# Optimization experiments

Hardware: AMD Instinct MI355X
Metric: run time of the kernel (lower is better)

Reference implementation:

```python
import jax, jax.numpy as jnp
from jax import lax
import numpy as np

D_MODEL, D_STATE, D_CONV, EXPAND = 192, 16, 3, 2
D_INNER = EXPAND * D_MODEL
B_, H_, W_ = 8, 128, 128
PAD = (D_CONV - 1) // 2
EPS = 1e-5


def setup_inputs() -> dict:
    key = jax.random.key(0)
    ks = jax.random.split(key, 8)
    s = 0.02
    return {
        "x": jax.random.normal(ks[0], (B_, D_MODEL, H_, W_), jnp.float32),
        "w_in": jax.random.normal(ks[1], (D_MODEL, 2 * D_INNER), jnp.float32) * s,
        "w_conv": jax.random.normal(ks[2], (D_INNER, 1, D_CONV, D_CONV), jnp.float32) * s,
        "b_conv": jnp.zeros((D_INNER,), jnp.float32),
        "w_x": jax.random.normal(ks[3], (D_INNER, 2 * D_STATE), jnp.float32) * s,
        "w_dt": jax.random.normal(ks[4], (D_STATE, D_INNER), jnp.float32) * s,
        "b_dt": jnp.zeros((D_INNER,), jnp.float32),
        "D_skip": jnp.ones((D_INNER,), jnp.float32),
        "w_out": jax.random.normal(ks[5], (D_INNER, D_MODEL), jnp.float32) * s,
        "gamma": jnp.ones((D_INNER,), jnp.float32),
        "beta": jnp.zeros((D_INNER,), jnp.float32),
    }


def _ss2d(x, w_in, w_conv, b_conv, w_x, w_dt, b_dt, D_skip, w_out, gamma, beta):
    B, C, H, W = x.shape
    L = H * W
    # NOTE: faithful to torch: x.reshape(B, H*W, C) on an NCHW tensor is a raw
    # row-major reinterpretation (same semantics as jnp.reshape), not a transpose.
    x_flat = x.reshape(B, L, C)
    x_proj = x_flat @ w_in                     # [B, L, 2*d_inner]
    x_inner, z = jnp.split(x_proj, 2, axis=-1)
    # depthwise conv over spatial dims
    xc = jnp.transpose(x_inner, (0, 2, 1)).reshape(B, D_INNER, H, W)
    xc = lax.conv_general_dilated(
        xc, w_conv, window_strides=(1, 1), padding=[(PAD, PAD), (PAD, PAD)],
        dimension_numbers=("NCHW", "OIHW", "NCHW"), feature_group_count=D_INNER,
    ) + b_conv[None, :, None, None]
    xc = jax.nn.silu(xc)
    xc = jnp.transpose(xc.reshape(B, D_INNER, L), (0, 2, 1))   # [B, L, d_inner]
    x_ssm = xc @ w_x                                            # [B, L, 2*d_state]
    B_ssm, C_ssm = jnp.split(x_ssm, 2, axis=-1)
    dt = jax.nn.softplus(B_ssm @ w_dt + b_dt)                   # [B, L, d_inner]
    # Original: deltaB = dt[...,None]*B_ssm[:,:,None,:]; einsum('blid,bld->bli', deltaB, C_ssm)
    # == dt * sum_d(B_ssm*C_ssm)  (deltaA is computed but never used -> dropped)
    bc = jnp.sum(B_ssm * C_ssm, axis=-1, keepdims=True)         # [B, L, 1]
    y = dt * bc + xc * D_skip                                   # [B, L, d_inner]
    y = y * jax.nn.silu(z)
    mu = jnp.mean(y, axis=-1, keepdims=True)
    var = jnp.mean(jnp.square(y - mu), axis=-1, keepdims=True)
    y = (y - mu) * lax.rsqrt(var + EPS) * gamma + beta
    out = y @ w_out                                             # [B, L, d_model]
    return jnp.transpose(out, (0, 2, 1)).reshape(B, C, H, W)


def reference(x, w_in, w_conv, b_conv, w_x, w_dt, b_dt, D_skip, w_out, gamma, beta):
    return _ss2d(x, w_in, w_conv, b_conv, w_x, w_dt, b_dt, D_skip, w_out, gamma, beta)
```

## Files before the change

kernel.cpp:

```cpp
#include <hip/hip_runtime.h>
#include <hip/hip_bf16.h>

typedef __bf16 bf16x8 __attribute__((ext_vector_type(8)));
typedef __bf16 bf16x4 __attribute__((ext_vector_type(4)));
typedef float  f32x4  __attribute__((ext_vector_type(4)));

__device__ __forceinline__ f32x4 mfma16(bf16x8 a, bf16x8 b, f32x4 c) {
    return __builtin_amdgcn_mfma_f32_16x16x32_bf16(a, b, c, 0, 0, 0);
}
__device__ __forceinline__ float silu_f(float v) { return v / (1.f + __expf(-v)); }
__device__ __forceinline__ float softplus_fast(float v) {
    float r = __logf(1.f + __expf(v));
    return v > 15.f ? v : r;
}

#define CC 192
#define DI 384
#define LL 16384
#define HH 128
#define WW 128

__global__ void k0_prep(const float* __restrict__ w_in, const float* __restrict__ w_x,
                        const float* __restrict__ w_dt, const float* __restrict__ w_out,
                        __bf16* __restrict__ wt_in, __bf16* __restrict__ wt_x,
                        __bf16* __restrict__ wt_dt, __bf16* __restrict__ wt_out) {
    int tid = blockIdx.x * blockDim.x + threadIdx.x;
    int nth = gridDim.x * blockDim.x;
    for (int i = tid; i < 768 * 192; i += nth) { int n = i / 192, k = i % 192; wt_in[i] = (__bf16)w_in[k * 768 + n]; }
    for (int i = tid; i < 32 * 384;  i += nth) { int n = i / 384, k = i % 384; wt_x[i]  = (__bf16)w_x[k * 32 + n]; }
    for (int i = tid; i < 384 * 16;  i += nth) { int ch = i / 16, k = i % 16;  wt_dt[i] = (__bf16)w_dt[k * 384 + ch]; }
    for (int i = tid; i < 192 * 384; i += nth) { int n = i / 384, k = i % 384; wt_out[i] = (__bf16)w_out[k * 192 + n]; }
}

__global__ __launch_bounds__(256, 4) void k1_proj(
        const float* __restrict__ x, const __bf16* __restrict__ wt_in,
        __bf16* __restrict__ xin, __bf16* __restrict__ zsb) {
    __shared__ __attribute__((aligned(16))) __bf16 wb[4 * 2 * 32 * 68];
    const int tid = threadIdx.x;
    const int lane = tid & 63, wv = tid >> 6;
    const int lq = lane & 15, quad = lane >> 4;
    const long mbase = (long)blockIdx.x * 128;
    __bf16* wbase = wb + wv * (2 * 32 * 68);

    bf16x8 af[2][6];
#pragma unroll
    for (int mt = 0; mt < 2; mt++) {
        const float* xr = x + (mbase + wv * 32 + mt * 16 + lq) * CC;
#pragma unroll
        for (int ks = 0; ks < 6; ks++) {
            float4 v0 = *(const float4*)(xr + ks * 32 + quad * 8);
            float4 v1 = *(const float4*)(xr + ks * 32 + quad * 8 + 4);
            bf16x8 t;
            t[0] = (__bf16)v0.x; t[1] = (__bf16)v0.y; t[2] = (__bf16)v0.z; t[3] = (__bf16)v0.w;
            t[4] = (__bf16)v1.x; t[5] = (__bf16)v1.y; t[6] = (__bf16)v1.z; t[7] = (__bf16)v1.w;
            af[mt][ks] = t;
        }
    }

    for (int nc = 0; nc < 12; nc++) {
        const __bf16* bnc = wt_in + (long)(nc * 64 + lq) * CC + quad * 8;
        f32x4 A0[4], A1[4];
#pragma unroll
        for (int nt = 0; nt < 4; nt++) {
            A0[nt] = (f32x4){0.f, 0.f, 0.f, 0.f};
            A1[nt] = (f32x4){0.f, 0.f, 0.f, 0.f};
        }
        bf16x8 bp[6];
#pragma unroll
        for (int i = 0; i < 6; i++)
            bp[i] = *(const bf16x8*)(bnc + (long)(i / 6) * 16 * CC + (i % 6) * 32);
#pragma unroll
        for (int i = 0; i < 24; i++) {
            const int nt = i / 6, ks = i % 6;
            bf16x8 bcur = bp[i % 6];
            const int i2 = i + 6;
            if (i2 < 24)
                bp[i % 6] = *(const bf16x8*)(bnc + (long)(i2 / 6) * 16 * CC + (i2 % 6) * 32);
            A0[nt] = mfma16(af[0][ks], bcur, A0[nt]);
            A1[nt] = mfma16(af[1][ks], bcur, A1[nt]);
        }
        const bool isz = (nc >= 6);
        __bf16* bb = wbase + (nc & 1) * (32 * 68);
#pragma unroll
        for (int nt = 0; nt < 4; nt++) {
#pragma unroll
            for (int r = 0; r < 4; r++) {
                float v0 = A0[nt][r], v1 = A1[nt][r];
                if (isz) { v0 = silu_f(v0); v1 = silu_f(v1); }
                bb[(quad * 4 + r) * 68 + nt * 16 + lq] = (__bf16)v0;
                bb[(16 + quad * 4 + r) * 68 + nt * 16 + lq] = (__bf16)v1;
            }
        }
        __builtin_amdgcn_wave_barrier();
        __bf16* dst = isz ? zsb : xin;
        const int chb = (isz ? nc - 6 : nc) * 64;
#pragma unroll
        for (int k = 0; k < 4; k++) {
            int u = lane + k * 64;
            int row = u >> 3, c8 = u & 7;
            unsigned long long lo = *(const unsigned long long*)(&bb[row * 68 + c8 * 8]);
            unsigned long long hi = *(const unsigned long long*)(&bb[row * 68 + c8 * 8 + 4]);
            ulonglong2 val; val.x = lo; val.y = hi;
            *(ulonglong2*)(dst + (mbase + wv * 32 + row) * DI + chb + c8 * 8) = val;
        }
        __builtin_amdgcn_wave_barrier();
    }
}

__global__ __launch_bounds__(256, 2) void k3_ssm(
        const __bf16* __restrict__ xin, const __bf16* __restrict__ zsb,
        const __bf16* __restrict__ wtx, const __bf16* __restrict__ wtdt,
        const __bf16* __restrict__ wtout, const float* __restrict__ wconv,
        const float* __restrict__ bconv, const float* __restrict__ bdt,
        const float* __restrict__ dskip, const float* __restrict__ gamma,
        const float* __restrict__ beta, float* __restrict__ out) {
    __shared__ __attribute__((aligned(16))) float smem0[13056];
    __shared__ __attribute__((aligned(16))) __bf16 dts[64 * 200];
    __shared__ __attribute__((aligned(16))) __bf16 bss[64 * 24];
    __shared__ float bcarr[64];
    __bf16* xcb = (__bf16*)smem0;
    float* otile = smem0;

    const int tid = threadIdx.x;
    const int lane = tid & 63, wv = tid >> 6;
    const int lq = lane & 15, quad = lane >> 4;
    const int t0g = blockIdx.x * 64;

    const int te = tid >> 2, part = tid & 3;
    const long tok = t0g + te;

    bf16x8 zpre[12];
#pragma unroll
    for (int h = 0; h < 2; h++)
#pragma unroll
        for (int g = 0; g < 6; g++)
            zpre[h * 6 + g] = *(const bf16x8*)(zsb + tok * DI + h * 192 + part * 48 + g * 8);

    float* wcvs = (float*)dts;
    float* bcvs = wcvs + 9 * 384;
    for (int u = tid; u < 9 * 384; u += 256) { int ch = u / 9, tap = u % 9; wcvs[tap * 384 + ch] = wconv[u]; }
    for (int u = tid; u < 384; u += 256) bcvs[u] = bconv[u];
    __syncthreads();

    const int hblk = (t0g & (LL - 1)) >> 7;
    const int w0 = t0g & 127;
#pragma unroll
    for (int k = 0; k < 12; k++) {
        int u = tid + k * 256;
        int t = u / 48, c8 = u % 48;
        long tk = t0g + t;
        float acc[8];
        float4 b0 = *(const float4*)(bcvs + c8 * 8);
        float4 b1 = *(const float4*)(bcvs + c8 * 8 + 4);
        acc[0] = b0.x; acc[1] = b0.y; acc[2] = b0.z; acc[3] = b0.w;
        acc[4] = b1.x; acc[5] = b1.y; acc[6] = b1.z; acc[7] = b1.w;
#pragma unroll
        for (int dy = -1; dy <= 1; dy++) {
            int h2 = hblk + dy;
            if (h2 < 0 || h2 >= HH) continue;
#pragma unroll
            for (int dx = -1; dx <= 1; dx++) {
                int w2 = w0 + t + dx;
                if (w2 < 0 || w2 >= WW) continue;
                bf16x8 v = *(const bf16x8*)(xin + (tk + dy * WW + dx) * (long)DI + c8 * 8);
                const float* wp = &wcvs[((dy + 1) * 3 + (dx + 1)) * 384 + c8 * 8];
#pragma unroll
                for (int j = 0; j < 8; j++) acc[j] += (float)v[j] * wp[j];
            }
        }
        bf16x8 r;
#pragma unroll
        for (int j = 0; j < 8; j++) r[j] = (__bf16)silu_f(acc[j]);
        *(bf16x8*)(&xcb[t * 392 + c8 * 8]) = r;
    }
    __syncthreads();

    {
        f32x4 aB = {0.f, 0.f, 0.f, 0.f}, aC = {0.f, 0.f, 0.f, 0.f};
#pragma unroll
        for (int ks = 0; ks < 12; ks++) {
            bf16x8 a = *(const bf16x8*)(&xcb[(wv * 16 + lq) * 392 + ks * 32 + quad * 8]);
            bf16x8 b0 = *(const bf16x8*)(wtx + lq * 384 + ks * 32 + quad * 8);
            bf16x8 b1 = *(const bf16x8*)(wtx + (16 + lq) * 384 + ks * 32 + quad * 8);
            aB = mfma16(a, b0, aB);
            aC = mfma16(a, b1, aC);
        }
        float p0 = aB[0] * aC[0], p1 = aB[1] * aC[1], p2 = aB[2] * aC[2], p3 = aB[3] * aC[3];
#pragma unroll
        for (int m = 1; m < 16; m <<= 1) {
            p0 += __shfl_xor(p0, m, 64);
            p1 += __shfl_xor(p1, m, 64);
            p2 += __shfl_xor(p2, m, 64);
            p3 += __shfl_xor(p3, m, 64);
        }
        int trow = wv * 16 + quad * 4;
        if (lq == 0) { bcarr[trow] = p0; bcarr[trow + 1] = p1; bcarr[trow + 2] = p2; bcarr[trow + 3] = p3; }
        bss[(trow + 0) * 24 + lq] = (__bf16)aB[0];
        bss[(trow + 1) * 24 + lq] = (__bf16)aB[1];
        bss[(trow + 2) * 24 + lq] = (__bf16)aB[2];
        bss[(trow + 3) * 24 + lq] = (__bf16)aB[3];
    }
    __syncthreads();

    bf16x8 zero8;
#pragma unroll
    for (int j = 0; j < 8; j++) zero8[j] = (__bf16)0.f;

    bf16x8 aA[4];
#pragma unroll
    for (int mt = 0; mt < 4; mt++)
        aA[mt] = (quad < 2) ? *(const bf16x8*)(&bss[(mt * 16 + lq) * 24 + quad * 8]) : zero8;

    float s1 = 0.f, s2 = 0.f;

#pragma unroll
    for (int h = 0; h < 2; h++) {
        f32x4 dacc[3][4];
        float bdtv[3];
#pragma unroll
        for (int j = 0; j < 3; j++) {
            int chg = h * 192 + (wv * 3 + j) * 16 + lq;
            bf16x8 bf = (quad < 2) ? *(const bf16x8*)(wtdt + (long)chg * 16 + quad * 8) : zero8;
            bdtv[j] = bdt[chg];
#pragma unroll
            for (int mt = 0; mt < 4; mt++) {
                f32x4 z4 = {0.f, 0.f, 0.f, 0.f};
                dacc[j][mt] = mfma16(aA[mt], bf, z4);
            }
        }
#pragma unroll
        for (int j = 0; j < 3; j++)
#pragma unroll
            for (int mt = 0; mt < 4; mt++)
#pragma unroll
                for (int r = 0; r < 4; r++)
                    dts[(mt * 16 + quad * 4 + r) * 200 + (wv * 3 + j) * 16 + lq] =
                        (__bf16)(dacc[j][mt][r] + bdtv[j]);
        __syncthreads();

#pragma unroll
        for (int g = 0; g < 6; g++) {
            const int chl = part * 48 + g * 8;
            const int chg = h * 192 + chl;
            bf16x8 d8 = *(const bf16x8*)(&dts[te * 200 + chl]);
            bf16x8 xc8 = *(const bf16x8*)(&xcb[te * 392 + chg]);
            bf16x8 z8 = zpre[h * 6 + g];
            float4 d0 = *(const float4*)(dskip + chg);
            float4 d1 = *(const float4*)(dskip + chg + 4);
            float ds[8] = {d0.x, d0.y, d0.z, d0.w, d1.x, d1.y, d1.z, d1.w};
            const float bcv = bcarr[te];
#pragma unroll
            for (int j = 0; j < 8; j++) {
                float dtv = softplus_fast((float)d8[j]);
                float yv = (dtv * bcv + (float)xc8[j] * ds[j]) * (float)z8[j];
                s1 += yv; s2 += yv * yv;
                xc8[j] = (__bf16)yv;
            }
            *(bf16x8*)(&xcb[te * 392 + chg]) = xc8;
        }
        __syncthreads();
    }

    {
        s1 += __shfl_xor(s1, 1, 64); s2 += __shfl_xor(s2, 1, 64);
        s1 += __shfl_xor(s1, 2, 64); s2 += __shfl_xor(s2, 2, 64);
        float mu = s1 * (1.f / 384.f);
        float var = s2 * (1.f / 384.f) - mu * mu;
        float rstd = rsqrtf(var + 1e-5f);
#pragma unroll
        for (int gg = 0; gg < 12; gg++) {
            const int h2 = gg / 6, g6 = gg % 6;
            const int ch = h2 * 192 + part * 48 + g6 * 8;
            bf16x8 v = *(const bf16x8*)(&xcb[te * 392 + ch]);
            float4 g0 = *(const float4*)(gamma + ch);
            float4 g1 = *(const float4*)(gamma + ch + 4);
            float4 be0 = *(const float4*)(beta + ch);
            float4 be1 = *(const float4*)(beta + ch + 4);
            float gm[8] = {g0.x, g0.y, g0.z, g0.w, g1.x, g1.y, g1.z, g1.w};
            float bt[8] = {be0.x, be0.y, be0.z, be0.w, be1.x, be1.y, be1.z, be1.w};
#pragma unroll
            for (int j = 0; j < 8; j++) v[j] = (__bf16)(((float)v[j] - mu) * rstd * gm[j] + bt[j]);
            *(bf16x8*)(&xcb[te * 392 + ch]) = v;
        }
    }
    __syncthreads();

    {
        f32x4 acc[3][4];
#pragma unroll
        for (int j = 0; j < 3; j++)
#pragma unroll
            for (int mt = 0; mt < 4; mt++) acc[j][mt] = (f32x4){0.f, 0.f, 0.f, 0.f};
#pragma unroll
        for (int ks = 0; ks < 12; ks++) {
            bf16x8 bfr[3];
#pragma unroll
            for (int j = 0; j < 3; j++) {
                int c = (wv * 3 + j) * 16 + lq;
                bfr[j] = *(const bf16x8*)(wtout + (long)c * 384 + ks * 32 + quad * 8);
            }
#pragma unroll
            for (int mt = 0; mt < 4; mt++) {
                bf16x8 afr = *(const bf16x8*)(&xcb[(mt * 16 + lq) * 392 + ks * 32 + quad * 8]);
#pragma unroll
                for (int j = 0; j < 3; j++) acc[j][mt] = mfma16(afr, bfr[j], acc[j][mt]);
            }
        }
        __syncthreads();
#pragma unroll
        for (int j = 0; j < 3; j++) {
            int c = (wv * 3 + j) * 16 + lq;
#pragma unroll
            for (int mt = 0; mt < 4; mt++)
#pragma unroll
                for (int r = 0; r < 4; r++)
                    otile[c * 68 + mt * 16 + quad * 4 + r] = acc[j][mt][r];
        }
    }
    __syncthreads();

    {
        const int bimg = t0g >> 14;
        const int l0 = t0g & (LL - 1);
#pragma unroll
        for (int k = 0; k < 12; k++) {
            int u = tid + k * 256;
            int c = u >> 4, j = u & 15;
            float4 v = *(const float4*)(&otile[c * 68 + j * 4]);
            *(float4*)(out + ((long)(bimg * CC + c)) * LL + l0 + j * 4) = v;
        }
    }
}

extern "C" void kernel_launch(void* const* d_in, const int* in_sizes, int n_in,
                              void* d_out, int out_size, void* d_ws, size_t ws_size,
                              hipStream_t stream) {
    (void)in_sizes; (void)n_in; (void)out_size; (void)ws_size;
    const float* x      = (const float*)d_in[0];
    const float* w_in   = (const float*)d_in[1];
    const float* w_conv = (const float*)d_in[2];
    const float* b_conv = (const float*)d_in[3];
    const float* w_x    = (const float*)d_in[4];
    const float* w_dt   = (const float*)d_in[5];
    const float* b_dt   = (const float*)d_in[6];
    const float* D_skip = (const float*)d_in[7];
    const float* w_out  = (const float*)d_in[8];
    const float* gamma  = (const float*)d_in[9];
    const float* beta   = (const float*)d_in[10];
    float* out = (float*)d_out;

    char* ws = (char*)d_ws;
    __bf16* wt_in  = (__bf16*)(ws);
    __bf16* wt_x   = (__bf16*)(ws + 294912);
    __bf16* wt_dt  = (__bf16*)(ws + 319488);
    __bf16* wt_out = (__bf16*)(ws + 331776);
    __bf16* xin    = (__bf16*)(ws + 479232);
    __bf16* zsb    = (__bf16*)(ws + 479232 + 100663296);

    k0_prep<<<96, 256, 0, stream>>>(w_in, w_x, w_dt, w_out, wt_in, wt_x, wt_dt, wt_out);
    k1_proj<<<1024, 256, 0, stream>>>(x, wt_in, xin, zsb);
    k3_ssm<<<2048, 256, 0, stream>>>(xin, zsb, wt_x, wt_dt, wt_out, w_conv, b_conv,
                                     b_dt, D_skip, gamma, beta, out);
}
```

Baseline: 551.5 us.

## Use 512-thread blocks in SSM kernel and simplify projection B-load loop

The fused SSM kernel now runs 8 waves per 64-token block instead of 4, and every phase is re-partitioned across them. The conv loop, elementwise work and output store are split 8 ways, and the x_proj, dt and out_proj MFMA tiles are redistributed, with B and C kept in fp32 LDS and reduced separately. The projection kernel drops its manual software-pipelined weight prefetch in favour of straightforward per-tile loads. This aims to raise latency hiding and wave occupancy per CU, at the cost of more syncs, tighter register limits from launch_bounds(512,4), and possibly less load/MFMA overlap in the projection.

```diff
diff --git a/kernel.cpp b/kernel.cpp
--- a/kernel.cpp
+++ b/kernel.cpp
@@ -58,26 +58,17 @@
     }
 
     for (int nc = 0; nc < 12; nc++) {
-        const __bf16* bnc = wt_in + (long)(nc * 64 + lq) * CC + quad * 8;
         f32x4 A0[4], A1[4];
 #pragma unroll
         for (int nt = 0; nt < 4; nt++) {
             A0[nt] = (f32x4){0.f, 0.f, 0.f, 0.f};
             A1[nt] = (f32x4){0.f, 0.f, 0.f, 0.f};
-        }
-        bf16x8 bp[6];
-#pragma unroll
-        for (int i = 0; i < 6; i++)
-            bp[i] = *(const bf16x8*)(bnc + (long)(i / 6) * 16 * CC + (i % 6) * 32);
-#pragma unroll
-        for (int i = 0; i < 24; i++) {
-            const int nt = i / 6, ks = i % 6;
-            bf16x8 bcur = bp[i % 6];
-            const int i2 = i + 6;
-            if (i2 < 24)
-                bp[i % 6] = *(const bf16x8*)(bnc + (long)(i2 / 6) * 16 * CC + (i2 % 6) * 32);
-            A0[nt] = mfma16(af[0][ks], bcur, A0[nt]);
-            A1[nt] = mfma16(af[1][ks], bcur, A1[nt]);
+#pragma unroll
+            for (int ks = 0; ks < 6; ks++) {
+                bf16x8 bf = *(const bf16x8*)(wt_in + (long)(nc * 64 + nt * 16 + lq) * CC + ks * 32 + quad * 8);
+                A0[nt] = mfma16(af[0][ks], bf, A0[nt]);
+                A1[nt] = mfma16(af[1][ks], bf, A1[nt]);
+            }
         }
         const bool isz = (nc >= 6);
         __bf16* bb = wbase + (nc & 1) * (32 * 68);
@@ -107,7 +98,7 @@
     }
 }
 
-__global__ __launch_bounds__(256, 2) void k3_ssm(
+__global__ __launch_bounds__(512, 4) void k3_ssm(
         const __bf16* __restrict__ xin, const __bf16* __restrict__ zsb,
         const __bf16* __restrict__ wtx, const __bf16* __restrict__ wtdt,
         const __bf16* __restrict__ wtout, const float* __restrict__ wconv,
@@ -116,7 +107,6 @@
         const float* __restrict__ beta, float* __restrict__ out) {
     __shared__ __attribute__((aligned(16))) float smem0[13056];
     __shared__ __attribute__((aligned(16))) __bf16 dts[64 * 200];
-    __shared__ __attribute__((aligned(16))) __bf16 bss[64 * 24];
     __shared__ float bcarr[64];
     __bf16* xcb = (__bf16*)smem0;
     float* otile = smem0;
@@ -126,27 +116,27 @@
     const int lq = lane & 15, quad = lane >> 4;
     const int t0g = blockIdx.x * 64;
 
-    const int te = tid >> 2, part = tid & 3;
+    const int te = tid >> 3, part = tid & 7;
     const long tok = t0g + te;
 
-    bf16x8 zpre[12];
+    bf16x8 zpre[6];
 #pragma unroll
     for (int h = 0; h < 2; h++)
 #pragma unroll
-        for (int g = 0; g < 6; g++)
-            zpre[h * 6 + g] = *(const bf16x8*)(zsb + tok * DI + h * 192 + part * 48 + g * 8);
+        for (int g = 0; g < 3; g++)
+            zpre[h * 3 + g] = *(const bf16x8*)(zsb + tok * DI + h * 192 + part * 24 + g * 8);
 
     float* wcvs = (float*)dts;
     float* bcvs = wcvs + 9 * 384;
-    for (int u = tid; u < 9 * 384; u += 256) { int ch = u / 9, tap = u % 9; wcvs[tap * 384 + ch] = wconv[u]; }
-    for (int u = tid; u < 384; u += 256) bcvs[u] = bconv[u];
+    for (int u = tid; u < 9 * 384; u += 512) { int ch = u / 9, tap = u % 9; wcvs[tap * 384 + ch] = wconv[u]; }
+    for (int u = tid; u < 384; u += 512) bcvs[u] = bconv[u];
     __syncthreads();
 
     const int hblk = (t0g & (LL - 1)) >> 7;
     const int w0 = t0g & 127;
 #pragma unroll
-    for (int k = 0; k < 12; k++) {
-        int u = tid + k * 256;
+    for (int k = 0; k < 6; k++) {
+        int u = tid + k * 512;
         int t = u / 48, c8 = u % 48;
         long tk = t0g + t;
         float acc[8];
@@ -175,76 +165,94 @@
     }
     __syncthreads();
 
-    {
-        f32x4 aB = {0.f, 0.f, 0.f, 0.f}, aC = {0.f, 0.f, 0.f, 0.f};
+    float* Bf = (float*)dts;
+    float* Cf = Bf + 64 * 20;
+    {
+        const int wt = wv & 3, wsel = wv >> 2;
+        f32x4 a4 = {0.f, 0.f, 0.f, 0.f};
 #pragma unroll
         for (int ks = 0; ks < 12; ks++) {
-            bf16x8 a = *(const bf16x8*)(&xcb[(wv * 16 + lq) * 392 + ks * 32 + quad * 8]);
-            bf16x8 b0 = *(const bf16x8*)(wtx + lq * 384 + ks * 32 + quad * 8);
-            bf16x8 b1 = *(const bf16x8*)(wtx + (16 + lq) * 384 + ks * 32 + quad * 8);
-            aB = mfma16(a, b0, aB);
-            aC = mfma16(a, b1, aC);
-        }
-        float p0 = aB[0] * aC[0], p1 = aB[1] * aC[1], p2 = aB[2] * aC[2], p3 = aB[3] * aC[3];
-#pragma unroll
-        for (int m = 1; m < 16; m <<= 1) {
-            p0 += __shfl_xor(p0, m, 64);
-            p1 += __shfl_xor(p1, m, 64);
-            p2 += __shfl_xor(p2, m, 64);
-            p3 += __shfl_xor(p3, m, 64);
-        }
-        int trow = wv * 16 + quad * 4;
-        if (lq == 0) { bcarr[trow] = p0; bcarr[trow + 1] = p1; bcarr[trow + 2] = p2; bcarr[trow + 3] = p3; }
-        bss[(trow + 0) * 24 + lq] = (__bf16)aB[0];
-        bss[(trow + 1) * 24 + lq] = (__bf16)aB[1];
-        bss[(trow + 2) * 24 + lq] = (__bf16)aB[2];
-        bss[(trow + 3) * 24 + lq] = (__bf16)aB[3];
-    }
-    __syncthreads();
-
+            bf16x8 a = *(const bf16x8*)(&xcb[(wt * 16 + lq) * 392 + ks * 32 + quad * 8]);
+            bf16x8 b = *(const bf16x8*)(wtx + (wsel * 16 + lq) * 384 + ks * 32 + quad * 8);
+            a4 = mfma16(a, b, a4);
+        }
+        float* dstf = wsel ? Cf : Bf;
+#pragma unroll
+        for (int r = 0; r < 4; r++)
+            dstf[(wt * 16 + quad * 4 + r) * 20 + lq] = a4[r];
+    }
+    __syncthreads();
+
+    {
+        int t = tid >> 3;
+        int s0 = (tid & 7) * 2;
+        float p = Bf[t * 20 + s0] * Cf[t * 20 + s0] + Bf[t * 20 + s0 + 1] * Cf[t * 20 + s0 + 1];
+        p += __shfl_xor(p, 1, 64);
+        p += __shfl_xor(p, 2, 64);
+        p += __shfl_xor(p, 4, 64);
+        if ((lane & 7) == 0) bcarr[t] = p;
+    }
     bf16x8 zero8;
 #pragma unroll
     for (int j = 0; j < 8; j++) zero8[j] = (__bf16)0.f;
-
     bf16x8 aA[4];
 #pragma unroll
-    for (int mt = 0; mt < 4; mt++)
-        aA[mt] = (quad < 2) ? *(const bf16x8*)(&bss[(mt * 16 + lq) * 24 + quad * 8]) : zero8;
+    for (int mt = 0; mt < 4; mt++) {
+        if (quad < 2) {
+            const float* bp = Bf + (mt * 16 + lq) * 20 + quad * 8;
+            f32x4 lo = *(const f32x4*)(bp);
+            f32x4 hi = *(const f32x4*)(bp + 4);
+            bf16x8 t8;
+            t8[0] = (__bf16)lo[0]; t8[1] = (__bf16)lo[1]; t8[2] = (__bf16)lo[2]; t8[3] = (__bf16)lo[3];
+            t8[4] = (__bf16)hi[0]; t8[5] = (__bf16)hi[1]; t8[6] = (__bf16)hi[2]; t8[7] = (__bf16)hi[3];
+            aA[mt] = t8;
+        } else {
+            aA[mt] = zero8;
+        }
+    }
+    __syncthreads();
 
     float s1 = 0.f, s2 = 0.f;
 
 #pragma unroll
     for (int h = 0; h < 2; h++) {
-        f32x4 dacc[3][4];
-        float bdtv[3];
-#pragma unroll
-        for (int j = 0; j < 3; j++) {
-            int chg = h * 192 + (wv * 3 + j) * 16 + lq;
-            bf16x8 bf = (quad < 2) ? *(const bf16x8*)(wtdt + (long)chg * 16 + quad * 8) : zero8;
-            bdtv[j] = bdt[chg];
-#pragma unroll
-            for (int mt = 0; mt < 4; mt++) {
-                f32x4 z4 = {0.f, 0.f, 0.f, 0.f};
-                dacc[j][mt] = mfma16(aA[mt], bf, z4);
-            }
-        }
-#pragma unroll
-        for (int j = 0; j < 3; j++)
-#pragma unroll
-            for (int mt = 0; mt < 4; mt++)
-#pragma unroll
-                for (int r = 0; r < 4; r++)
-                    dts[(mt * 16 + quad * 4 + r) * 200 + (wv * 3 + j) * 16 + lq] =
-                        (__bf16)(dacc[j][mt][r] + bdtv[j]);
+        f32x4 dacc[2][4];
+        float bdtv[2];
+#pragma unroll
+        for (int j = 0; j < 2; j++) {
+            const int tile = wv + 8 * j;
+            if (tile < 12) {
+                int chg = h * 192 + tile * 16 + lq;
+                bf16x8 bf = (quad < 2) ? *(const bf16x8*)(wtdt + (long)chg * 16 + quad * 8) : zero8;
+                bdtv[j] = bdt[chg];
+#pragma unroll
+                for (int mt = 0; mt < 4; mt++) {
+                    f32x4 z4 = {0.f, 0.f, 0.f, 0.f};
+                    dacc[j][mt] = mfma16(aA[mt], bf, z4);
+                }
+            }
+        }
+#pragma unroll
+        for (int j = 0; j < 2; j++) {
+            const int tile = wv + 8 * j;
+            if (tile < 12) {
+#pragma unroll
+                for (int mt = 0; mt < 4; mt++)
+#pragma unroll
+                    for (int r = 0; r < 4; r++)
+                        dts[(mt * 16 + quad * 4 + r) * 200 + tile * 16 + lq] =
+                            (__bf16)(dacc[j][mt][r] + bdtv[j]);
+            }
+        }
         __syncthreads();
 
 #pragma unroll
-        for (int g = 0; g < 6; g++) {
-            const int chl = part * 48 + g * 8;
+        for (int g = 0; g < 3; g++) {
+            const int chl = part * 24 + g * 8;
             const int chg = h * 192 + chl;
             bf16x8 d8 = *(const bf16x8*)(&dts[te * 200 + chl]);
             bf16x8 xc8 = *(const bf16x8*)(&xcb[te * 392 + chg]);
-            bf16x8 z8 = zpre[h * 6 + g];
+            bf16x8 z8 = zpre[h * 3 + g];
             float4 d0 = *(const float4*)(dskip + chg);
             float4 d1 = *(const float4*)(dskip + chg + 4);
             float ds[8] = {d0.x, d0.y, d0.z, d0.w, d1.x, d1.y, d1.z, d1.w};
@@ -264,13 +272,14 @@
     {
         s1 += __shfl_xor(s1, 1, 64); s2 += __shfl_xor(s2, 1, 64);
         s1 += __shfl_xor(s1, 2, 64); s2 += __shfl_xor(s2, 2, 64);
+        s1 += __shfl_xor(s1, 4, 64); s2 += __shfl_xor(s2, 4, 64);
         float mu = s1 * (1.f / 384.f);
         float var = s2 * (1.f / 384.f) - mu * mu;
         float rstd = rsqrtf(var + 1e-5f);
 #pragma unroll
-        for (int gg = 0; gg < 12; gg++) {
-            const int h2 = gg / 6, g6 = gg % 6;
-            const int ch = h2 * 192 + part * 48 + g6 * 8;
+        for (int gg = 0; gg < 6; gg++) {
+            const int h2 = gg / 3, g3 = gg % 3;
+            const int ch = h2 * 192 + part * 24 + g3 * 8;
             bf16x8 v = *(const bf16x8*)(&xcb[te * 392 + ch]);
             float4 g0 = *(const float4*)(gamma + ch);
             float4 g1 = *(const float4*)(gamma + ch + 4);
@@ -286,35 +295,36 @@
     __syncthreads();
 
     {
-        f32x4 acc[3][4];
+        const int mh = wv >> 2, nb = (wv & 3) * 3;
+        f32x4 acc[3][2];
 #pragma unroll
         for (int j = 0; j < 3; j++)
 #pragma unroll
-            for (int mt = 0; mt < 4; mt++) acc[j][mt] = (f32x4){0.f, 0.f, 0.f, 0.f};
+            for (int m2 = 0; m2 < 2; m2++) acc[j][m2] = (f32x4){0.f, 0.f, 0.f, 0.f};
 #pragma unroll
         for (int ks = 0; ks < 12; ks++) {
             bf16x8 bfr[3];
 #pragma unroll
             for (int j = 0; j < 3; j++) {
-                int c = (wv * 3 + j) * 16 + lq;
+                int c = (nb + j) * 16 + lq;
                 bfr[j] = *(const bf16x8*)(wtout + (long)c * 384 + ks * 32 + quad * 8);
             }
 #pragma unroll
-            for (int mt = 0; mt < 4; mt++) {
-                bf16x8 afr = *(const bf16x8*)(&xcb[(mt * 16 + lq) * 392 + ks * 32 + quad * 8]);
-#pragma unroll
-                for (int j = 0; j < 3; j++) acc[j][mt] = mfma16(afr, bfr[j], acc[j][mt]);
+            for (int m2 = 0; m2 < 2; m2++) {
+                bf16x8 afr = *(const bf16x8*)(&xcb[((mh * 2 + m2) * 16 + lq) * 392 + ks * 32 + quad * 8]);
+#pragma unroll
+                for (int j = 0; j < 3; j++) acc[j][m2] = mfma16(afr, bfr[j], acc[j][m2]);
             }
         }
         __syncthreads();
 #pragma unroll
         for (int j = 0; j < 3; j++) {
-            int c = (wv * 3 + j) * 16 + lq;
-#pragma unroll
-            for (int mt = 0; mt < 4; mt++)
+            int c = (nb + j) * 16 + lq;
+#pragma unroll
+            for (int m2 = 0; m2 < 2; m2++)
 #pragma unroll
                 for (int r = 0; r < 4; r++)
-                    otile[c * 68 + mt * 16 + quad * 4 + r] = acc[j][mt][r];
+                    otile[c * 68 + (mh * 2 + m2) * 16 + quad * 4 + r] = acc[j][m2][r];
         }
     }
     __syncthreads();
@@ -323,8 +333,8 @@
         const int bimg = t0g >> 14;
         const int l0 = t0g & (LL - 1);
 #pragma unroll
-        for (int k = 0; k < 12; k++) {
-            int u = tid + k * 256;
+        for (int k = 0; k < 6; k++) {
+            int u = tid + k * 512;
             int c = u >> 4, j = u & 15;
             float4 v = *(const float4*)(&otile[c * 68 + j * 4]);
             *(float4*)(out + ((long)(bimg * CC + c)) * LL + l0 + j * 4) = v;
@@ -359,6 +369,6 @@
 
     k0_prep<<<96, 256, 0, stream>>>(w_in, w_x, w_dt, w_out, wt_in, wt_x, wt_dt, wt_out);
     k1_proj<<<1024, 256, 0, stream>>>(x, wt_in, xin, zsb);
-    k3_ssm<<<2048, 256, 0, stream>>>(xin, zsb, wt_x, wt_dt, wt_out, w_conv, b_conv,
+    k3_ssm<<<2048, 512, 0, stream>>>(xin, zsb, wt_x, wt_dt, wt_out, w_conv, b_conv,
                                      b_dt, D_skip, gamma, beta, out);
 }
```

New measurement: 561.2 us. About the same (+1.8%).

## Stage input-projection weights into LDS with async double-buffered loads

Applied to the files above, without the earlier changes.

The input-projection kernel now copies each 64-column chunk of the bf16 weight matrix into shared memory with global_load_lds, double-buffered across chunks. Previously every wave read the weights straight from global memory. The prep kernel writes the weights in a chunked, XOR-swizzled layout so the LDS reads avoid bank conflicts. This adds about 48KB of LDS and a block-wide barrier per chunk, and lowers the occupancy hint from 4 to 2. The cost it targets is redundant per-wave global weight traffic.

```diff
diff --git a/kernel.cpp b/kernel.cpp
--- a/kernel.cpp
+++ b/kernel.cpp
@@ -26,21 +26,27 @@
                         __bf16* __restrict__ wt_dt, __bf16* __restrict__ wt_out) {
     int tid = blockIdx.x * blockDim.x + threadIdx.x;
     int nth = gridDim.x * blockDim.x;
-    for (int i = tid; i < 768 * 192; i += nth) { int n = i / 192, k = i % 192; wt_in[i] = (__bf16)w_in[k * 768 + n]; }
+    for (int i = tid; i < 768 * 192; i += nth) {
+        int nf = i / 192, k = i % 192;
+        int nc = nf >> 6, n = nf & 63;
+        int e = (n * 192 + k) ^ ((n & 7) << 3);
+        wt_in[nc * 12288 + e] = (__bf16)w_in[k * 768 + nf];
+    }
     for (int i = tid; i < 32 * 384;  i += nth) { int n = i / 384, k = i % 384; wt_x[i]  = (__bf16)w_x[k * 32 + n]; }
     for (int i = tid; i < 384 * 16;  i += nth) { int ch = i / 16, k = i % 16;  wt_dt[i] = (__bf16)w_dt[k * 384 + ch]; }
     for (int i = tid; i < 192 * 384; i += nth) { int n = i / 384, k = i % 384; wt_out[i] = (__bf16)w_out[k * 192 + n]; }
 }
 
-__global__ __launch_bounds__(256, 4) void k1_proj(
+__global__ __launch_bounds__(256, 2) void k1_proj(
         const float* __restrict__ x, const __bf16* __restrict__ wt_in,
         __bf16* __restrict__ xin, __bf16* __restrict__ zsb) {
-    __shared__ __attribute__((aligned(16))) __bf16 wb[4 * 2 * 32 * 68];
+    __shared__ __attribute__((aligned(16))) __bf16 Bs[2][12288];
+    __shared__ __attribute__((aligned(16))) __bf16 bounce[4][32 * 68];
     const int tid = threadIdx.x;
     const int lane = tid & 63, wv = tid >> 6;
     const int lq = lane & 15, quad = lane >> 4;
     const long mbase = (long)blockIdx.x * 128;
-    __bf16* wbase = wb + wv * (2 * 32 * 68);
+    __bf16* bb = &bounce[wv][0];
 
     bf16x8 af[2][6];
 #pragma unroll
@@ -57,30 +63,41 @@
         }
     }
 
+    auto stage = [&](int b, int nc) {
+        const char* src = (const char*)(wt_in + nc * 12288);
+        char* dst = (char*)&Bs[b][0];
+#pragma unroll
+        for (int i = 0; i < 6; i++) {
+            int off = (wv * 6 + i) * 1024;
+            __builtin_amdgcn_global_load_lds(
+                (const __attribute__((address_space(1))) void*)(src + off + lane * 16),
+                (__attribute__((address_space(3))) void*)(dst + off),
+                16, 0, 0);
+        }
+    };
+
+    stage(0, 0);
+    __syncthreads();
+
+    int buf = 0;
     for (int nc = 0; nc < 12; nc++) {
-        const __bf16* bnc = wt_in + (long)(nc * 64 + lq) * CC + quad * 8;
+        if (nc < 11) stage(buf ^ 1, nc + 1);
+
         f32x4 A0[4], A1[4];
 #pragma unroll
         for (int nt = 0; nt < 4; nt++) {
             A0[nt] = (f32x4){0.f, 0.f, 0.f, 0.f};
             A1[nt] = (f32x4){0.f, 0.f, 0.f, 0.f};
-        }
-        bf16x8 bp[6];
-#pragma unroll
-        for (int i = 0; i < 6; i++)
-            bp[i] = *(const bf16x8*)(bnc + (long)(i / 6) * 16 * CC + (i % 6) * 32);
-#pragma unroll
-        for (int i = 0; i < 24; i++) {
-            const int nt = i / 6, ks = i % 6;
-            bf16x8 bcur = bp[i % 6];
-            const int i2 = i + 6;
-            if (i2 < 24)
-                bp[i % 6] = *(const bf16x8*)(bnc + (long)(i2 / 6) * 16 * CC + (i2 % 6) * 32);
-            A0[nt] = mfma16(af[0][ks], bcur, A0[nt]);
-            A1[nt] = mfma16(af[1][ks], bcur, A1[nt]);
+#pragma unroll
+            for (int ks = 0; ks < 6; ks++) {
+                const int row = nt * 16 + lq;
+                const int e = (row * 192 + ks * 32 + quad * 8) ^ ((lq & 7) << 3);
+                bf16x8 bf = *(const bf16x8*)(&Bs[buf][e]);
+                A0[nt] = mfma16(af[0][ks], bf, A0[nt]);
+                A1[nt] = mfma16(af[1][ks], bf, A1[nt]);
+            }
         }
         const bool isz = (nc >= 6);
-        __bf16* bb = wbase + (nc & 1) * (32 * 68);
 #pragma unroll
         for (int nt = 0; nt < 4; nt++) {
 #pragma unroll
@@ -103,7 +120,8 @@
             ulonglong2 val; val.x = lo; val.y = hi;
             *(ulonglong2*)(dst + (mbase + wv * 32 + row) * DI + chb + c8 * 8) = val;
         }
-        __builtin_amdgcn_wave_barrier();
+        __syncthreads();
+        buf ^= 1;
     }
 }
 
```

Measured after the change: 488.0 us. 1.13x faster.
